# Kernel tuning notes

Measured on AMD Instinct MI355X. Metric: run time of the kernel, lower is better.

The kernel has to match this reference:

```python
import jax, jax.numpy as jnp
import numpy as np

SIGMA_MIN, SIGMA_MAX = 0.03, 0.35
LAMBDA_GEO = 8.0
COMPAT_SCALE = 0.1
INVALID_W = 0.05
NH, HD = 8, 64
LN_EPS = 1e-5

def _ln(x, g, b):
    m = x.mean(-1, keepdims=True)
    v = ((x - m) ** 2).mean(-1, keepdims=True)
    return (x - m) * jax.lax.rsqrt(v + LN_EPS) * g + b

def setup_inputs() -> dict:
    key = jax.random.key(0)
    ks = jax.random.split(key, 32)
    B, C, H, W = 8, 512, 32, 32
    T, S, D, SIN = 1024, 1024, 512, 512
    s = 0.02
    inp = {
        'front_feat': jax.random.normal(ks[0], (B, C, H, W), jnp.float32),
        'sat_tokens': jax.random.normal(ks[1], (B, S, SIN), jnp.float32),
        'sat_xy': jax.random.uniform(ks[2], (B, S, 2), jnp.float32),
        'front_bev_xy': jax.random.uniform(ks[3], (B, T, 2), jnp.float32),
        'front_bev_valid_mask': jax.random.bernoulli(ks[4], 0.9, (B, T)),
        'front_plucker': jax.random.normal(ks[5], (B, T, 6), jnp.float32),
        'fa_w': jax.random.normal(ks[6], (C, D), jnp.float32) * s,
        'fa_b': jnp.zeros((D,), jnp.float32),
        'fa_g': jnp.ones((D,), jnp.float32),
        'fa_lb': jnp.zeros((D,), jnp.float32),
        'sa_w': jax.random.normal(ks[7], (SIN, D), jnp.float32) * s,
        'sa_b': jnp.zeros((D,), jnp.float32),
        'sa_g': jnp.ones((D,), jnp.float32),
        'sa_lb': jnp.zeros((D,), jnp.float32),
        'q_w': jax.random.normal(ks[8], (D, D), jnp.float32) * s,
        'q_b': jnp.zeros((D,), jnp.float32),
        'k_w': jax.random.normal(ks[9], (D, D), jnp.float32) * s,
        'k_b': jnp.zeros((D,), jnp.float32),
        'v_w': jax.random.normal(ks[10], (D, D), jnp.float32) * s,
        'v_b': jnp.zeros((D,), jnp.float32),
        'pl_w1': jax.random.normal(ks[11], (6, D), jnp.float32) * s,
        'pl_b1': jnp.zeros((D,), jnp.float32),
        'pl_w2': jax.random.normal(ks[12], (D, D), jnp.float32) * s,
        'pl_b2': jnp.zeros((D,), jnp.float32),
        'sig_w': jax.random.normal(ks[13], (D, 1), jnp.float32) * s,
        'sig_b': jnp.zeros((1,), jnp.float32),
        'db_w': jax.random.normal(ks[14], (D, NH), jnp.float32) * s,
        'db_b': jnp.zeros((NH,), jnp.float32),
        'out_w': jax.random.normal(ks[15], (D, C), jnp.float32) * s,
        'out_b': jnp.zeros((C,), jnp.float32),
    }
    return inp

def _forward(front_feat, sat_tokens, sat_xy, front_bev_xy, front_plucker,
             fa_w, fa_b, fa_g, fa_lb, sa_w, sa_b, sa_g, sa_lb,
             q_w, q_b, k_w, k_b, v_w, v_b, pl_w1, pl_b1, pl_w2, pl_b2,
             sig_w, sig_b, db_w, db_b, out_w, out_b, valid_mask):
    B, C, H, W = front_feat.shape
    T = H * W
    D = NH * HD
    front_flat = front_feat.reshape(B, C, T).transpose(0, 2, 1)  # [B,T,C]
    front_embed = _ln(front_flat @ fa_w + fa_b, fa_g, fa_lb)
    pl = jax.nn.silu(front_plucker @ pl_w1 + pl_b1) @ pl_w2 + pl_b2
    context = front_embed + pl
    sat_embed = _ln(sat_tokens @ sa_w + sa_b, sa_g, sa_lb)
    def heads(x):
        return x.reshape(B, -1, NH, HD).transpose(0, 2, 1, 3)  # [B,H,N,d]
    q = heads(front_embed @ q_w + q_b)
    k = heads(sat_embed @ k_w + k_b)
    v = heads(sat_embed @ v_w + v_b)
    compat = jnp.einsum('bhtd,bhsd->bhts', q, k) / jnp.sqrt(jnp.float32(HD))
    compat = COMPAT_SCALE * compat
    sigma = SIGMA_MIN + (SIGMA_MAX - SIGMA_MIN) * jax.nn.sigmoid((context @ sig_w + sig_b)[..., 0])  # [B,T]
    dist2 = ((front_bev_xy[:, :, None, :] - sat_xy[:, None, :, :]) ** 2).sum(-1)  # [B,T,S]
    geo = -LAMBDA_GEO * dist2 / jnp.maximum(sigma[..., None] ** 2, 1e-6)
    sat_logits = compat + geo[:, None]  # [B,H,T,S]
    sat_logits = jnp.where(valid_mask[:, None, :, None], sat_logits, jnp.float32(-10000.0))
    dustbin = (context @ db_w + db_b).transpose(0, 2, 1)[..., None]  # [B,H,T,1]
    logits = jnp.concatenate([sat_logits, dustbin], axis=-1)
    probs = jax.nn.softmax(logits, axis=-1)
    sat_probs, dustbin_prob = probs[..., :-1], probs[..., -1]
    read = jnp.einsum('bhts,bhsd->bhtd', sat_probs, v)
    read = read.transpose(0, 2, 1, 3).reshape(B, T, D)
    read_feat = (read @ out_w + out_b).transpose(0, 2, 1).reshape(B, C, H, W)
    confidence = (1.0 - dustbin_prob).mean(axis=1)  # [B,T]
    conf_feat = confidence.reshape(B, 1, H, W)
    front_feat_out = front_feat + conf_feat * read_feat
    vf = valid_mask.astype(confidence.dtype)
    inv = 1.0 - vf
    invalid_conf = (confidence * inv).sum() / jnp.maximum(inv.sum(), 1.0)
    invalid_conf_loss = invalid_conf * INVALID_W
    return front_feat_out, read_feat, confidence, invalid_conf_loss

def reference(front_feat, sat_tokens, sat_xy, front_bev_xy, front_bev_valid_mask, front_plucker,
              fa_w, fa_b, fa_g, fa_lb, sa_w, sa_b, sa_g, sa_lb,
              q_w, q_b, k_w, k_b, v_w, v_b, pl_w1, pl_b1, pl_w2, pl_b2,
              sig_w, sig_b, db_w, db_b, out_w, out_b):
    return _forward(front_feat, sat_tokens, sat_xy, front_bev_xy, front_plucker,
                    fa_w, fa_b, fa_g, fa_lb, sa_w, sa_b, sa_g, sa_lb,
                    q_w, q_b, k_w, k_b, v_w, v_b, pl_w1, pl_b1, pl_w2, pl_b2,
                    sig_w, sig_b, db_w, db_b, out_w, out_b, front_bev_valid_mask)
```

## Files before the change

kernel.cpp:

```cpp
#include <hip/hip_runtime.h>

typedef unsigned short u16;
typedef __attribute__((ext_vector_type(8))) short short8;
typedef __attribute__((ext_vector_type(4))) float f32x4;

constexpr int B_  = 8;
constexpr int C_  = 512;
constexpr int T_  = 1024;
constexpr int S_  = 1024;
constexpr int D_  = 512;
constexpr int NH_ = 8;
constexpr int BT_ = B_ * T_;
constexpr float INVLN2 = 1.44269504088896340736f;
constexpr float QSCALE2 = 0.0125f * INVLN2;

__device__ __forceinline__ unsigned pack2(float lo, float hi) {
    unsigned r;
    asm("v_cvt_pk_bf16_f32 %0, %1, %2" : "=v"(r) : "v"(lo), "v"(hi));
    return r;
}
__device__ __forceinline__ u16 f2bf(float x) {
    return (u16)pack2(x, x);
}
__device__ __forceinline__ float bf2f(u16 h) {
    union { unsigned u; float f; } v; v.u = ((unsigned)h) << 16;
    return v.f;
}
__device__ __forceinline__ float fexp2(float x) {
    float r;
    asm("v_exp_f32 %0, %1" : "=v"(r) : "v"(x));
    return r;
}
__device__ __forceinline__ float max3f(float a, float b, float c) {
    float r;
    asm("v_max3_f32 %0, %1, %2, %3" : "=v"(r) : "v"(a), "v"(b), "v"(c));
    return r;
}

#define GWAITBAR(N) do { \
    asm volatile("s_waitcnt vmcnt(" #N ") lgkmcnt(0)" ::: "memory"); \
    __builtin_amdgcn_sched_barrier(0); \
    __builtin_amdgcn_s_barrier(); \
    __builtin_amdgcn_sched_barrier(0); } while (0)

typedef __attribute__((address_space(3))) unsigned int lds_u32;
typedef const __attribute__((address_space(1))) unsigned int glob_u32;
__device__ __forceinline__ void g2l16(void* l, const void* g) {
    __builtin_amdgcn_global_load_lds((glob_u32*)g, (lds_u32*)l, 16, 0, 0);
}

__device__ __forceinline__ int is_valid(const void* mask, int mode, int idx) {
    if (mode == 0) return ((const int*)mask)[idx] != 0;
    if (mode == 1) return ((const float*)mask)[idx] != 0.0f;
    return ((const unsigned char*)mask)[idx] != 0;
}

__global__ __launch_bounds__(256) void prep_k(
    const float* __restrict__ ff, const float* __restrict__ sat,
    const float* __restrict__ pl,
    const float* a0, const float* a1, const float* a2, const float* a3,
    const float* a4, const float* a5, u16* __restrict__ WT,
    u16* __restrict__ ffb, u16* __restrict__ satb,
    const float* __restrict__ plw1, const float* __restrict__ plb1,
    u16* __restrict__ plh,
    const unsigned* __restrict__ maskw, int* __restrict__ mode,
    float* __restrict__ scal,
    const float* __restrict__ plw2, const float* __restrict__ sigw,
    const float* __restrict__ dbw, const float* __restrict__ plb2,
    float* __restrict__ wsig, float* __restrict__ wdbfT,
    float* __restrict__ offs, float* __restrict__ dbwT) {
    __shared__ float tile[32][33];
    int blk = blockIdx.x, tid = threadIdx.x;
    if (blk < 4096) {
        int t0 = (blk & 31) * 32, c0 = ((blk >> 5) & 15) * 32, b = blk >> 9;
        int tx = tid & 31, ty = tid >> 5;
        const float* ip = ff + (size_t)b * C_ * T_;
        for (int i = ty; i < 32; i += 8)
            tile[i][tx] = ip[(size_t)(c0 + i) * T_ + t0 + tx];
        __syncthreads();
        u16* op = ffb + (size_t)b * T_ * C_;
        for (int i = ty; i < 32; i += 8)
            op[(size_t)(t0 + i) * C_ + c0 + tx] = f2bf(tile[tx][i]);
    } else if (blk < 5632) {
        int idx = blk - 4096;
        const float* srcs[6] = {a0, a1, a2, a3, a4, a5};
        int z = idx >> 8;
        const float* src = srcs[z];
        u16* d = WT + (size_t)z * 512 * 512;
        int k0 = (idx & 15) * 32, n0 = ((idx >> 4) & 15) * 32;
        int tx = tid & 31, ty = tid >> 5;
        for (int i = ty; i < 32; i += 8)
            tile[i][tx] = src[(size_t)(k0 + i) * 512 + n0 + tx];
        __syncthreads();
        for (int i = ty; i < 32; i += 8)
            d[(size_t)(n0 + i) * 512 + k0 + tx] = f2bf(tile[tx][i]);
    } else if (blk < 7680) {
        int i = (blk - 5632) * 256 + tid;
        const float4* p = (const float4*)(sat + (size_t)i * 8);
        float4 a = p[0], b = p[1];
        uint4 o;
        o.x = pack2(a.x, a.y); o.y = pack2(a.z, a.w);
        o.z = pack2(b.x, b.y); o.w = pack2(b.z, b.w);
        *(uint4*)(satb + (size_t)i * 8) = o;
    } else if (blk < 9728) {
        int m = (blk - 7680) * 4 + (tid >> 6);
        int lane = tid & 63;
        float p6[6];
#pragma unroll
        for (int j = 0; j < 6; ++j) p6[j] = pl[(size_t)m * 6 + j];
        int n0 = lane * 8;
        float acc[8];
#pragma unroll
        for (int e = 0; e < 8; ++e) acc[e] = plb1[n0 + e];
#pragma unroll
        for (int j = 0; j < 6; ++j) {
            float4 wv0 = *(const float4*)(plw1 + j * D_ + n0);
            float4 wv1 = *(const float4*)(plw1 + j * D_ + n0 + 4);
            acc[0] += p6[j] * wv0.x; acc[1] += p6[j] * wv0.y;
            acc[2] += p6[j] * wv0.z; acc[3] += p6[j] * wv0.w;
            acc[4] += p6[j] * wv1.x; acc[5] += p6[j] * wv1.y;
            acc[6] += p6[j] * wv1.z; acc[7] += p6[j] * wv1.w;
        }
        uint4 o;
        float s0 = acc[0] / (1.0f + __expf(-acc[0]));
        float s1 = acc[1] / (1.0f + __expf(-acc[1]));
        float s2 = acc[2] / (1.0f + __expf(-acc[2]));
        float s3 = acc[3] / (1.0f + __expf(-acc[3]));
        float s4 = acc[4] / (1.0f + __expf(-acc[4]));
        float s5 = acc[5] / (1.0f + __expf(-acc[5]));
        float s6 = acc[6] / (1.0f + __expf(-acc[6]));
        float s7 = acc[7] / (1.0f + __expf(-acc[7]));
        o.x = pack2(s0, s1); o.y = pack2(s2, s3);
        o.z = pack2(s4, s5); o.w = pack2(s6, s7);
        *(uint4*)(plh + (size_t)m * D_ + n0) = o;
    } else if (blk == 9728) {
        __shared__ int bad_i, bad_f;
        if (tid == 0) { bad_i = 0; bad_f = 0; }
        __syncthreads();
        for (int i = tid; i < 2048; i += 256) {
            unsigned v = maskw[i];
            if (v > 1u) bad_i = 1;
            if (v != 0u && v != 0x3f800000u) bad_f = 1;
        }
        __syncthreads();
        if (tid == 0) {
            *mode = (!bad_i) ? 0 : ((!bad_f) ? 1 : 2);
            scal[0] = 0.0f; scal[1] = 0.0f;
        }
    } else if (blk < 9731) {
        int k = (blk - 9729) * 256 + tid;
        const float* wr = plw2 + (size_t)k * 512;
        float acc = 0;
        for (int n = 0; n < 512; n += 4) {
            float4 wv = *(const float4*)(wr + n);
            float4 sv = *(const float4*)(sigw + n);
            acc += wv.x * sv.x + wv.y * sv.y + wv.z * sv.z + wv.w * sv.w;
        }
        wsig[k] = acc;
    } else if (blk < 9747) {
        int idx = blk - 9731;
        int k = idx * 32 + (tid >> 3), h = tid & 7;
        const float* wr = plw2 + (size_t)k * 512;
        float acc = 0;
        for (int n = 0; n < 512; ++n) acc += wr[n] * dbw[n * 8 + h];
        wdbfT[h * 512 + k] = acc;
    } else if (blk == 9747) {
        float p = plb2[tid] * sigw[tid] + plb2[tid + 256] * sigw[tid + 256];
        float ph[8];
#pragma unroll
        for (int h = 0; h < 8; ++h)
            ph[h] = plb2[tid] * dbw[tid * 8 + h] +
                    plb2[tid + 256] * dbw[(tid + 256) * 8 + h];
        for (int o = 32; o; o >>= 1) {
            p += __shfl_down(p, o);
#pragma unroll
            for (int h = 0; h < 8; ++h) ph[h] += __shfl_down(ph[h], o);
        }
        __shared__ float red[4][9];
        int wv = tid >> 6, lane = tid & 63;
        if (lane == 0) {
            red[wv][0] = p;
#pragma unroll
            for (int h = 0; h < 8; ++h) red[wv][1 + h] = ph[h];
        }
        __syncthreads();
        if (tid == 0) {
            for (int j = 0; j < 9; ++j) {
                float t = 0;
                for (int v2 = 0; v2 < 4; ++v2) t += red[v2][j];
                offs[j] = t;
            }
        }
    } else {
        for (int i = tid; i < 4096; i += 256) {
            int h = i >> 9, n = i & 511;
            dbwT[h * 512 + n] = dbw[n * 8 + h];
        }
    }
}

__global__ __launch_bounds__(256) void gmm_k(
    const u16* __restrict__ A0, const u16* __restrict__ A1,
    const u16* __restrict__ A2, const u16* __restrict__ A3,
    const u16* __restrict__ Bt0, const u16* __restrict__ Bt1,
    const u16* __restrict__ Bt2, const u16* __restrict__ Bt3,
    const float* __restrict__ bb0, const float* __restrict__ bb1,
    const float* __restrict__ bb2, const float* __restrict__ bb3,
    void* __restrict__ C0v, void* __restrict__ C1v,
    void* __restrict__ C2v, void* __restrict__ C3v,
    int md0, int md1, int md2, int md3,
    const u16* __restrict__ addend,
    const float* __restrict__ ffp, float* __restrict__ out1p,
    const float* __restrict__ dbpp, const void* __restrict__ maskp,
    const int* __restrict__ modep, float* __restrict__ outcp,
    float* __restrict__ scalp) {
    __shared__ u16 As[3][4096];
    __shared__ u16 Bs[3][4096];
    __shared__ float confL[128];
    int jid = blockIdx.x >> 8;
    int L = blockIdx.x & 255;
    const u16* A    = (jid == 0) ? A0 : (jid == 1) ? A1 : (jid == 2) ? A2 : A3;
    const u16* Bt   = (jid == 0) ? Bt0 : (jid == 1) ? Bt1 : (jid == 2) ? Bt2 : Bt3;
    const float* bias = (jid == 0) ? bb0 : (jid == 1) ? bb1 : (jid == 2) ? bb2 : bb3;
    void* Cv        = (jid == 0) ? C0v : (jid == 1) ? C1v : (jid == 2) ? C2v : C3v;
    int mode        = (jid == 0) ? md0 : (jid == 1) ? md1 : (jid == 2) ? md2 : md3;

    int tid = threadIdx.x, w = tid >> 6, l = tid & 63;
    int lr = l & 15, g = l >> 4;
    int W = (L & 7) * 32 + (L >> 3);
    int m0 = (W >> 2) * 128, n0 = (W & 3) * 128;
    int wr = w >> 1, wc = w & 1;
    int prm = g ^ ((lr >> 1) & 3);

    f32x4 acc[4][4] = {};

    if (mode == 4 && tid < 128) {
        int row = m0 + tid;
        const float* dr = dbpp + (size_t)row * NH_;
        float s = 0;
#pragma unroll
        for (int h = 0; h < 8; ++h) s += dr[h];
        float cf = 1.0f - s * 0.125f;
        confL[tid] = cf;
        if ((W & 3) == 0) {
            outcp[row] = cf;
            int md = *modep;
            float invd = is_valid(maskp, md, row) ? 0.0f : 1.0f;
            float a = cf * invd, bsum = invd;
            for (int o = 32; o; o >>= 1) {
                a += __shfl_down(a, o);
                bsum += __shfl_down(bsum, o);
            }
            if ((tid & 63) == 0) {
                atomicAdd(&scalp[0], a);
                atomicAdd(&scalp[1], bsum);
            }
        }
    }

    auto stage = [&](int buf, int k0) {
#pragma unroll
        for (int j = 0; j < 2; ++j) {
            int i = tid + 256 * j;
            int row = i >> 2, gg = (i & 3) ^ ((i >> 3) & 3);
            g2l16((char*)As[buf] + (size_t)i * 16,
                  A + (size_t)(m0 + row) * 512 + k0 + gg * 8);
        }
#pragma unroll
        for (int j = 0; j < 2; ++j) {
            int i = tid + 256 * j;
            int col = i >> 2, gg = (i & 3) ^ ((i >> 3) & 3);
            g2l16((char*)Bs[buf] + (size_t)i * 16,
                  Bt + (size_t)(n0 + col) * 512 + k0 + gg * 8);
        }
    };

    auto compute = [&](int bi) {
        const char* Ab = (const char*)As[bi];
        const char* Bb = (const char*)Bs[bi];
        short8 af[4], bf[4];
#pragma unroll
        for (int m = 0; m < 4; ++m)
            af[m] = *(const short8*)(Ab + ((wr * 64 + m * 16 + lr) * 4 + prm) * 16);
#pragma unroll
        for (int n = 0; n < 4; ++n)
            bf[n] = *(const short8*)(Bb + ((wc * 64 + n * 16 + lr) * 4 + prm) * 16);
        __builtin_amdgcn_s_setprio(1);
#pragma unroll
        for (int m = 0; m < 4; ++m)
#pragma unroll
            for (int n = 0; n < 4; ++n)
                acc[m][n] = __builtin_amdgcn_mfma_f32_16x16x32_bf16(
                    af[m], bf[n], acc[m][n], 0, 0, 0);
        __builtin_amdgcn_s_setprio(0);
    };

    stage(0, 0);
    stage(1, 32);
    for (int t = 0; t < 14; ++t) {
        stage((t + 2) % 3, (t + 2) * 32);
        GWAITBAR(8);
        compute(t % 3);
        __builtin_amdgcn_s_barrier();
    }
    GWAITBAR(4);
    compute(2);
    GWAITBAR(0);
    compute(0);

    float bs[4];
#pragma unroll
    for (int n = 0; n < 4; ++n) bs[n] = bias[n0 + wc * 64 + n * 16 + lr];

#pragma unroll
    for (int m = 0; m < 4; ++m) {
#pragma unroll
        for (int n = 0; n < 4; ++n) {
            int R0  = m0 + wr * 64 + m * 16 + 4 * g;
            int col = n0 + wc * 64 + n * 16 + lr;
            if (mode == 3) {
                int bbx = R0 >> 10, ss = R0 & 1023, hh = col >> 6, dd = col & 63;
                uint2 pk;
                pk.x = pack2(acc[m][n][0] + bs[n], acc[m][n][1] + bs[n]);
                pk.y = pack2(acc[m][n][2] + bs[n], acc[m][n][3] + bs[n]);
                u16* dst = (u16*)Cv + ((size_t)(bbx * 8 + hh) * 64 + dd) * 1024 + ss;
                *(uint2*)dst = pk;
            } else if (mode == 4) {
                int bbx = R0 >> 10, t0p = R0 & 1023;
                size_t base = (size_t)bbx * C_ * T_ + (size_t)col * T_ + t0p;
                float4 rf;
                rf.x = acc[m][n][0] + bs[n]; rf.y = acc[m][n][1] + bs[n];
                rf.z = acc[m][n][2] + bs[n]; rf.w = acc[m][n][3] + bs[n];
                float4 ffv = *(const float4*)(ffp + base);
                float4 cfv = *(const float4*)&confL[R0 - m0];
                float4 o0v;
                o0v.x = ffv.x + cfv.x * rf.x; o0v.y = ffv.y + cfv.y * rf.y;
                o0v.z = ffv.z + cfv.z * rf.z; o0v.w = ffv.w + cfv.w * rf.w;
                *(float4*)(out1p + base) = rf;
                *(float4*)((float*)Cv + base) = o0v;
            } else {
#pragma unroll
                for (int j = 0; j < 4; ++j) {
                    int row = R0 + j;
                    float v = acc[m][n][j] + bs[n];
                    if (mode == 1) v *= QSCALE2;
                    if (mode == 2) v += bf2f(addend[(size_t)row * 512 + col]);
                    ((u16*)Cv)[(size_t)row * 512 + col] = f2bf(v);
                }
            }
        }
    }
}

__global__ __launch_bounds__(256) void ln2_k(
    const u16* __restrict__ X0, const float* __restrict__ g0,
    const float* __restrict__ b0, u16* __restrict__ O0,
    const u16* __restrict__ X1, const float* __restrict__ g1,
    const float* __restrict__ b1, u16* __restrict__ O1) {
    int sel = blockIdx.x >> 13;
    int row = blockIdx.x & 8191;
    const u16* X = sel ? X1 : X0;
    const float* gw = sel ? g1 : g0;
    const float* bw = sel ? b1 : b0;
    u16* out = sel ? O1 : O0;
    int tid = threadIdx.x;
    const unsigned* xr = (const unsigned*)(X + (size_t)row * D_);
    unsigned u = xr[tid];
    float x0 = bf2f((u16)(u & 0xffff)), x1 = bf2f((u16)(u >> 16));
    float s = x0 + x1, sq = x0 * x0 + x1 * x1;
    __shared__ float rs[4], rq[4];
    for (int o = 32; o; o >>= 1) { s += __shfl_down(s, o); sq += __shfl_down(sq, o); }
    int wid = tid >> 6, lane = tid & 63;
    if (lane == 0) { rs[wid] = s; rq[wid] = sq; }
    __syncthreads();
    if (tid == 0) {
        float ts = 0, tq = 0;
        for (int w = 0; w < 4; ++w) { ts += rs[w]; tq += rq[w]; }
        rs[0] = ts; rq[0] = tq;
    }
    __syncthreads();
    float mean = rs[0] * (1.0f / D_);
    float var  = rq[0] * (1.0f / D_) - mean * mean;
    float r = rsqrtf(var + 1e-5f);
    float2 g2 = *(const float2*)(gw + 2 * tid);
    float2 b2 = *(const float2*)(bw + 2 * tid);
    float y0 = (x0 - mean) * r * g2.x + b2.x;
    float y1 = (x1 - mean) * r * g2.y + b2.y;
    ((unsigned*)(out + (size_t)row * D_))[tid] = pack2(y0, y1);
}

__global__ __launch_bounds__(256) void head2_k(
    const u16* __restrict__ E, const u16* __restrict__ PLH,
    const float* __restrict__ sigw, const float* __restrict__ sigb,
    const float* __restrict__ wsig, const float* __restrict__ dbwT,
    const float* __restrict__ wdbfT, const float* __restrict__ dbb,
    const float* __restrict__ offs,
    float* __restrict__ sigma, float* __restrict__ dbo) {
    int wv = threadIdx.x >> 6, lane = threadIdx.x & 63;
    int row = blockIdx.x * 4 + wv;
    uint4 ue = *((const uint4*)(E + (size_t)row * 512) + lane);
    float Ev[8];
    Ev[0] = bf2f((u16)(ue.x & 0xffff)); Ev[1] = bf2f((u16)(ue.x >> 16));
    Ev[2] = bf2f((u16)(ue.y & 0xffff)); Ev[3] = bf2f((u16)(ue.y >> 16));
    Ev[4] = bf2f((u16)(ue.z & 0xffff)); Ev[5] = bf2f((u16)(ue.z >> 16));
    Ev[6] = bf2f((u16)(ue.w & 0xffff)); Ev[7] = bf2f((u16)(ue.w >> 16));
    uint4 up = *((const uint4*)(PLH + (size_t)row * 512) + lane);
    float plv[8];
    plv[0] = bf2f((u16)(up.x & 0xffff)); plv[1] = bf2f((u16)(up.x >> 16));
    plv[2] = bf2f((u16)(up.y & 0xffff)); plv[3] = bf2f((u16)(up.y >> 16));
    plv[4] = bf2f((u16)(up.z & 0xffff)); plv[5] = bf2f((u16)(up.z >> 16));
    plv[6] = bf2f((u16)(up.w & 0xffff)); plv[7] = bf2f((u16)(up.w >> 16));

    int n0 = lane * 8;
    float4 sw0 = *(const float4*)(sigw + n0);
    float4 sw1 = *(const float4*)(sigw + n0 + 4);
    float4 fw0 = *(const float4*)(wsig + n0);
    float4 fw1 = *(const float4*)(wsig + n0 + 4);
    float swv[8] = {sw0.x, sw0.y, sw0.z, sw0.w, sw1.x, sw1.y, sw1.z, sw1.w};
    float fwv[8] = {fw0.x, fw0.y, fw0.z, fw0.w, fw1.x, fw1.y, fw1.z, fw1.w};
    float sacc = 0;
#pragma unroll
    for (int i = 0; i < 8; ++i) sacc += Ev[i] * swv[i] + plv[i] * fwv[i];

    float d_[8];
#pragma unroll
    for (int h = 0; h < 8; ++h) {
        const float* ar = dbwT + h * 512 + n0;
        const float* br = wdbfT + h * 512 + n0;
        float4 a0v = *(const float4*)ar;
        float4 a1v = *(const float4*)(ar + 4);
        float4 b0v = *(const float4*)br;
        float4 b1v = *(const float4*)(br + 4);
        d_[h] = Ev[0] * a0v.x + Ev[1] * a0v.y + Ev[2] * a0v.z + Ev[3] * a0v.w +
                Ev[4] * a1v.x + Ev[5] * a1v.y + Ev[6] * a1v.z + Ev[7] * a1v.w +
                plv[0] * b0v.x + plv[1] * b0v.y + plv[2] * b0v.z + plv[3] * b0v.w +
                plv[4] * b1v.x + plv[5] * b1v.y + plv[6] * b1v.z + plv[7] * b1v.w;
    }
    for (int o = 1; o < 64; o <<= 1) {
        sacc += __shfl_xor(sacc, o);
#pragma unroll
        for (int h = 0; h < 8; ++h) d_[h] += __shfl_xor(d_[h], o);
    }
    if (lane == 0) {
        float z = sacc + sigb[0] + offs[0];
        sigma[row] = 0.03f + 0.32f / (1.0f + __expf(-z));
        float* dd = dbo + (size_t)row * NH_;
#pragma unroll
        for (int h = 0; h < 8; ++h) dd[h] = d_[h] + dbb[h] + offs[1 + h];
    }
}

__global__ __launch_bounds__(512) void attn_k(
    const u16* __restrict__ Q, const u16* __restrict__ K,
    const u16* __restrict__ Vt, const float* __restrict__ sig,
    const float* __restrict__ dbl, const float* __restrict__ bev,
    const float* __restrict__ sxy, const void* __restrict__ mask,
    const int* __restrict__ mode, u16* __restrict__ OUT,
    float* __restrict__ dbp) {
    int L = blockIdx.x;
    int W = (L & 7) * 64 + (L >> 3);
    int b = W >> 6, h = (W >> 3) & 7, tblk = W & 7;
    int tid = threadIdx.x, w = tid >> 6, l = tid & 63;
    int lr = l & 15, g = l >> 4;
    int p8 = lr & 7;

    __shared__ u16 Kbuf[2][4096];
    __shared__ u16 Vbuf[2][4096];
    __shared__ float2 SXY[1024];
    __shared__ float  SZ[1024];

    const float2* xp = (const float2*)(sxy + (size_t)b * S_ * 2);
#pragma unroll
    for (int j = 0; j < 2; ++j) {
        int idx = tid + 512 * j;
        float2 v = xp[idx];
        SXY[idx] = make_float2(-2.0f * v.x, -2.0f * v.y);
        SZ[idx] = v.x * v.x + v.y * v.y;
    }

    int trow = b * T_ + tblk * 128 + w * 16 + lr;
    float s_ = sig[trow];
    float bx = bev[(size_t)trow * 2], by = bev[(size_t)trow * 2 + 1];
    float dbv2 = dbl[(size_t)trow * NH_ + h] * INVLN2;
    int md = *mode;
    bool vld = is_valid(mask, md, trow) != 0;
    float grow  = vld ? (-11.5415603271117f / fmaxf(s_ * s_, 1e-6f)) : 0.0f;
    float Abase = vld ? grow * (bx * bx + by * by) : -10000.0f;
    float AbaseM = Abase - dbv2;
    float mshift = 0.0f;

    const u16* qp = Q + (size_t)trow * 512 + h * 64 + g * 8;
    short8 q0 = *(const short8*)qp;
    short8 q1 = *(const short8*)(qp + 32);
    if (!vld) { q0 = short8{}; q1 = short8{}; }

    short8 ones;
#pragma unroll
    for (int e = 0; e < 8; ++e) ones[e] = (short)0x3F80;

    const u16* Kp = K + (size_t)b * S_ * 512 + h * 64;
    const u16* Vp = Vt + (size_t)(b * 8 + h) * 64 * 1024;

    int srow = tid >> 3;
    int gprm = (tid & 7) ^ (srow & 7);
    int sK = ((srow >> 5) & 1) * 32 + ((srow >> 2) & 3) * 8 +
             ((srow >> 4) & 1) * 4 + (srow & 3);

    auto stageKV = [&](int buf, int s0) {
        g2l16((char*)Kbuf[buf] + (size_t)tid * 16,
              Kp + (size_t)(s0 + sK) * 512 + gprm * 8);
        g2l16((char*)Vbuf[buf] + (size_t)tid * 16,
              Vp + (size_t)srow * 1024 + s0 + gprm * 8);
    };

    f32x4 o0 = {}, o1 = {}, o2 = {}, o3 = {};
    f32x4 o4 = {1.0f, 1.0f, 1.0f, 1.0f};

    stageKV(0, 0);
    int cur = 0;
    for (int c = 0; c < 16; ++c) {
        int s0c = c * 64;
        if (c < 15) {
            stageKV(cur ^ 1, s0c + 64);
            GWAITBAR(2);
        } else {
            GWAITBAR(0);
        }

        const char* Kc = (const char*)Kbuf[cur];
        const char* Vc = (const char*)Vbuf[cur];

        f32x4 p[4];
        f32x4 z4 = {};
        __builtin_amdgcn_s_setprio(1);
#pragma unroll
        for (int sub = 0; sub < 4; ++sub) {
            int krow = sub * 16 + lr;
            short8 kf0 = *(const short8*)(Kc + (krow * 8 + (g ^ p8)) * 16);
            short8 kf1 = *(const short8*)(Kc + (krow * 8 + ((4 + g) ^ p8)) * 16);
            p[sub] = __builtin_amdgcn_mfma_f32_16x16x32_bf16(kf0, q0, z4, 0, 0, 0);
            p[sub] = __builtin_amdgcn_mfma_f32_16x16x32_bf16(kf1, q1, p[sub], 0, 0, 0);
        }
        __builtin_amdgcn_s_setprio(0);

        float lg[16];
#pragma unroll
        for (int sub = 0; sub < 4; ++sub) {
            int sl = s0c + ((sub & 2) << 4) + 8 * g + ((sub & 1) << 2);
            float4 xy01 = *(const float4*)&SXY[sl];
            float4 xy23 = *(const float4*)&SXY[sl + 2];
            float4 zz   = *(const float4*)&SZ[sl];
            float X[4] = {xy01.x, xy01.z, xy23.x, xy23.z};
            float Y[4] = {xy01.y, xy01.w, xy23.y, xy23.w};
            float Z[4] = {zz.x, zz.y, zz.z, zz.w};
#pragma unroll
            for (int i2 = 0; i2 < 4; ++i2) {
                float wg = fmaf(bx, X[i2], fmaf(by, Y[i2], Z[i2]));
                lg[sub * 4 + i2] = fmaf(grow, wg, p[sub][i2] + AbaseM);
            }
        }
        float c0 = max3f(lg[0], lg[1], lg[2]);
        float c1 = max3f(lg[3], lg[4], lg[5]);
        float c2 = max3f(lg[6], lg[7], lg[8]);
        float c3 = max3f(lg[9], lg[10], lg[11]);
        float c4 = max3f(lg[12], lg[13], lg[14]);
        float cl = fmaxf(max3f(c0, c1, c2), max3f(c3, c4, lg[15]));

        if (!__all(cl <= 11.5f)) {
            cl = fmaxf(cl, __shfl_xor(cl, 16));
            cl = fmaxf(cl, __shfl_xor(cl, 32));
            float dm = fmaxf(cl, 0.0f);
            float scl = fexp2(-dm);
            o0 *= scl; o1 *= scl; o2 *= scl; o3 *= scl; o4 *= scl;
            AbaseM -= dm;
            mshift -= dm;
#pragma unroll
            for (int r = 0; r < 16; ++r) lg[r] -= dm;
        }
        float pe[16];
#pragma unroll
        for (int r = 0; r < 16; ++r) pe[r] = fexp2(lg[r]);

        union { uint4 u; short8 s8; } pf0, pf1;
        pf0.u.x = pack2(pe[0], pe[1]);  pf0.u.y = pack2(pe[2], pe[3]);
        pf0.u.z = pack2(pe[4], pe[5]);  pf0.u.w = pack2(pe[6], pe[7]);
        pf1.u.x = pack2(pe[8], pe[9]);  pf1.u.y = pack2(pe[10], pe[11]);
        pf1.u.z = pack2(pe[12], pe[13]); pf1.u.w = pack2(pe[14], pe[15]);

        __builtin_amdgcn_s_setprio(1);
        short8 vf;
#pragma unroll
        for (int dt = 0; dt < 4; ++dt) {
            int vrow = dt * 16 + lr;
            f32x4* oo = (dt == 0) ? &o0 : (dt == 1) ? &o1 : (dt == 2) ? &o2 : &o3;
            vf = *(const short8*)(Vc + (vrow * 8 + (g ^ p8)) * 16);
            *oo = __builtin_amdgcn_mfma_f32_16x16x32_bf16(vf, pf0.s8, *oo, 0, 0, 0);
            vf = *(const short8*)(Vc + (vrow * 8 + ((4 + g) ^ p8)) * 16);
            *oo = __builtin_amdgcn_mfma_f32_16x16x32_bf16(vf, pf1.s8, *oo, 0, 0, 0);
        }
        o4 = __builtin_amdgcn_mfma_f32_16x16x32_bf16(ones, pf0.s8, o4, 0, 0, 0);
        o4 = __builtin_amdgcn_mfma_f32_16x16x32_bf16(ones, pf1.s8, o4, 0, 0, 0);
        __builtin_amdgcn_s_setprio(0);

        __builtin_amdgcn_s_barrier();
        cur ^= 1;
    }

    float inv = 1.0f / o4[0];
    u16* ob = OUT + (size_t)trow * 512 + h * 64;
    {
        uint2 pk;
        pk.x = pack2(o0[0] * inv, o0[1] * inv); pk.y = pack2(o0[2] * inv, o0[3] * inv);
        *(uint2*)(ob + 0 * 16 + 4 * g) = pk;
        pk.x = pack2(o1[0] * inv, o1[1] * inv); pk.y = pack2(o1[2] * inv, o1[3] * inv);
        *(uint2*)(ob + 1 * 16 + 4 * g) = pk;
        pk.x = pack2(o2[0] * inv, o2[1] * inv); pk.y = pack2(o2[2] * inv, o2[3] * inv);
        *(uint2*)(ob + 2 * 16 + 4 * g) = pk;
        pk.x = pack2(o3[0] * inv, o3[1] * inv); pk.y = pack2(o3[2] * inv, o3[3] * inv);
        *(uint2*)(ob + 3 * 16 + 4 * g) = pk;
    }
    if (g == 0) dbp[(size_t)trow * NH_ + h] = fexp2(mshift) * inv;
}

__global__ void loss_k(const float* __restrict__ scal, float* __restrict__ out) {
    out[0] = scal[0] / fmaxf(scal[1], 1.0f) * 0.05f;
}

extern "C" void kernel_launch(void* const* d_in, const int* in_sizes, int n_in,
                              void* d_out, int out_size, void* d_ws, size_t ws_size,
                              hipStream_t stream) {
    const float* front_feat = (const float*)d_in[0];
    const float* sat_tokens = (const float*)d_in[1];
    const float* sat_xy     = (const float*)d_in[2];
    const float* bev_xy     = (const float*)d_in[3];
    const void*  mask       = d_in[4];
    const float* plucker    = (const float*)d_in[5];
    const float* fa_w = (const float*)d_in[6];
    const float* fa_b = (const float*)d_in[7];
    const float* fa_g = (const float*)d_in[8];
    const float* fa_lb = (const float*)d_in[9];
    const float* sa_w = (const float*)d_in[10];
    const float* sa_b = (const float*)d_in[11];
    const float* sa_g = (const float*)d_in[12];
    const float* sa_lb = (const float*)d_in[13];
    const float* q_w = (const float*)d_in[14];
    const float* q_b = (const float*)d_in[15];
    const float* k_w = (const float*)d_in[16];
    const float* k_b = (const float*)d_in[17];
    const float* v_w = (const float*)d_in[18];
    const float* v_b = (const float*)d_in[19];
    const float* pl_w1 = (const float*)d_in[20];
    const float* pl_b1 = (const float*)d_in[21];
    const float* pl_w2 = (const float*)d_in[22];
    const float* pl_b2 = (const float*)d_in[23];
    const float* sig_w = (const float*)d_in[24];
    const float* sig_b = (const float*)d_in[25];
    const float* db_w = (const float*)d_in[26];
    const float* db_b = (const float*)d_in[27];
    const float* out_w = (const float*)d_in[28];
    const float* out_b = (const float*)d_in[29];

    char* w8 = (char*)d_ws;
    u16* H0 = (u16*)(w8);
    u16* H1 = (u16*)(w8 + 8388608ull * 1);
    u16* H2 = (u16*)(w8 + 8388608ull * 2);
    u16* H3 = (u16*)(w8 + 8388608ull * 3);
    u16* H4 = (u16*)(w8 + 8388608ull * 4);
    u16* H5 = (u16*)(w8 + 8388608ull * 5);
    u16* H6 = (u16*)(w8 + 8388608ull * 6);
    u16* WT = (u16*)(w8 + 8388608ull * 7);
    char* sm = w8 + 8388608ull * 7 + 3670016ull;
    float* w_sigma = (float*)sm;
    float* w_db    = w_sigma + BT_;
    float* w_dbp   = w_db + (size_t)BT_ * NH_;
    float* w_scal  = w_dbp + (size_t)BT_ * NH_;
    int*   w_mode  = (int*)(w_scal + 2);
    float* w_wsig  = w_scal + 4;
    float* w_wdbfT = w_wsig + 512;
    float* w_offs  = w_wdbfT + 4096;
    float* w_dbwT  = w_offs + 16;

    u16* Wfa = WT;                 u16* Wq  = WT + 262144ull * 1;
    u16* Wsa = WT + 262144ull * 2; u16* Wk  = WT + 262144ull * 3;
    u16* Wv  = WT + 262144ull * 4; u16* Wo  = WT + 262144ull * 5;

    float* out0 = (float*)d_out;
    float* out1 = out0 + (size_t)B_ * C_ * T_;
    float* outc = out1 + (size_t)B_ * C_ * T_;
    float* outl = outc + (size_t)B_ * T_;

    dim3 blk(256);

    prep_k<<<dim3(9749), blk, 0, stream>>>(
        front_feat, sat_tokens, plucker,
        fa_w, q_w, sa_w, k_w, v_w, out_w, WT,
        H0, H5, pl_w1, pl_b1, H2,
        (const unsigned*)mask, w_mode, w_scal,
        pl_w2, sig_w, db_w, pl_b2, w_wsig, w_wdbfT, w_offs, w_dbwT);
    gmm_k<<<dim3(512), blk, 0, stream>>>(
        H0, H5, nullptr, nullptr,
        Wfa, Wsa, nullptr, nullptr,
        fa_b, sa_b, nullptr, nullptr,
        H6, H4, nullptr, nullptr,
        0, 0, 0, 0,
        nullptr, nullptr, nullptr,
        nullptr, nullptr, nullptr, nullptr, nullptr);
    ln2_k<<<dim3(16384), blk, 0, stream>>>(H6, fa_g, fa_lb, H1,
                                           H4, sa_g, sa_lb, H3);
    head2_k<<<dim3(2048), blk, 0, stream>>>(
        H1, H2, sig_w, sig_b, w_wsig, w_dbwT, w_wdbfT, db_b, w_offs,
        w_sigma, w_db);
    gmm_k<<<dim3(768), blk, 0, stream>>>(
        H1, H3, H3, nullptr,
        Wq, Wk, Wv, nullptr,
        q_b, k_b, v_b, nullptr,
        H5, H0, H4, nullptr,
        1, 0, 3, 0,
        nullptr, nullptr, nullptr,
        nullptr, nullptr, nullptr, nullptr, nullptr);
    attn_k<<<dim3(512), dim3(512), 0, stream>>>(
        H5, H0, H4, w_sigma, w_db, bev_xy, sat_xy, mask, w_mode, H2, w_dbp);
    gmm_k<<<dim3(256), blk, 0, stream>>>(
        H2, nullptr, nullptr, nullptr,
        Wo, nullptr, nullptr, nullptr,
        out_b, nullptr, nullptr, nullptr,
        out0, nullptr, nullptr, nullptr,
        4, 0, 0, 0,
        nullptr, front_feat, out1,
        w_dbp, mask, w_mode, outc, w_scal);
    loss_k<<<1, 1, 0, stream>>>(w_scal, outl);
}
```

Before: 156.6 us.

## Fuse head projection into LayerNorm and split output GEMM into narrower tiles

The sigma and dustbin head computation is folded into the LayerNorm kernel, so the normalized front features are used directly from registers instead of being reread by a separate head kernel, and one launch is dropped. The final output projection moves from the generic GEMM kernel to a dedicated kernel with 128x64 tiles and 512 blocks, doubling the block count to fill more compute units. In exchange, each LN block gains extra reductions and a barrier, and the narrower tiles reread A more often. The generic GEMM loses its unused mode-2 and mode-4 paths.

Result: no change. 159.7 us (+2.0%).

```diff
diff --git a/kernel.cpp b/kernel.cpp
--- a/kernel.cpp
+++ b/kernel.cpp
@@ -201,29 +201,22 @@
 
 __global__ __launch_bounds__(256) void gmm_k(
     const u16* __restrict__ A0, const u16* __restrict__ A1,
-    const u16* __restrict__ A2, const u16* __restrict__ A3,
+    const u16* __restrict__ A2,
     const u16* __restrict__ Bt0, const u16* __restrict__ Bt1,
-    const u16* __restrict__ Bt2, const u16* __restrict__ Bt3,
+    const u16* __restrict__ Bt2,
     const float* __restrict__ bb0, const float* __restrict__ bb1,
-    const float* __restrict__ bb2, const float* __restrict__ bb3,
-    void* __restrict__ C0v, void* __restrict__ C1v,
-    void* __restrict__ C2v, void* __restrict__ C3v,
-    int md0, int md1, int md2, int md3,
-    const u16* __restrict__ addend,
-    const float* __restrict__ ffp, float* __restrict__ out1p,
-    const float* __restrict__ dbpp, const void* __restrict__ maskp,
-    const int* __restrict__ modep, float* __restrict__ outcp,
-    float* __restrict__ scalp) {
+    const float* __restrict__ bb2,
+    void* __restrict__ C0v, void* __restrict__ C1v, void* __restrict__ C2v,
+    int md0, int md1, int md2) {
     __shared__ u16 As[3][4096];
     __shared__ u16 Bs[3][4096];
-    __shared__ float confL[128];
     int jid = blockIdx.x >> 8;
     int L = blockIdx.x & 255;
-    const u16* A    = (jid == 0) ? A0 : (jid == 1) ? A1 : (jid == 2) ? A2 : A3;
-    const u16* Bt   = (jid == 0) ? Bt0 : (jid == 1) ? Bt1 : (jid == 2) ? Bt2 : Bt3;
-    const float* bias = (jid == 0) ? bb0 : (jid == 1) ? bb1 : (jid == 2) ? bb2 : bb3;
-    void* Cv        = (jid == 0) ? C0v : (jid == 1) ? C1v : (jid == 2) ? C2v : C3v;
-    int mode        = (jid == 0) ? md0 : (jid == 1) ? md1 : (jid == 2) ? md2 : md3;
+    const u16* A    = (jid == 0) ? A0 : (jid == 1) ? A1 : A2;
+    const u16* Bt   = (jid == 0) ? Bt0 : (jid == 1) ? Bt1 : Bt2;
+    const float* bias = (jid == 0) ? bb0 : (jid == 1) ? bb1 : bb2;
+    void* Cv        = (jid == 0) ? C0v : (jid == 1) ? C1v : C2v;
+    int mode        = (jid == 0) ? md0 : (jid == 1) ? md1 : md2;
 
     int tid = threadIdx.x, w = tid >> 6, l = tid & 63;
     int lr = l & 15, g = l >> 4;
@@ -234,7 +227,107 @@
 
     f32x4 acc[4][4] = {};
 
-    if (mode == 4 && tid < 128) {
+    auto stage = [&](int buf, int k0) {
+#pragma unroll
+        for (int j = 0; j < 2; ++j) {
+            int i = tid + 256 * j;
+            int row = i >> 2, gg = (i & 3) ^ ((i >> 3) & 3);
+            g2l16((char*)As[buf] + (size_t)i * 16,
+                  A + (size_t)(m0 + row) * 512 + k0 + gg * 8);
+        }
+#pragma unroll
+        for (int j = 0; j < 2; ++j) {
+            int i = tid + 256 * j;
+            int col = i >> 2, gg = (i & 3) ^ ((i >> 3) & 3);
+            g2l16((char*)Bs[buf] + (size_t)i * 16,
+                  Bt + (size_t)(n0 + col) * 512 + k0 + gg * 8);
+        }
+    };
+
+    auto compute = [&](int bi) {
+        const char* Ab = (const char*)As[bi];
+        const char* Bb = (const char*)Bs[bi];
+        short8 af[4], bf[4];
+#pragma unroll
+        for (int m = 0; m < 4; ++m)
+            af[m] = *(const short8*)(Ab + ((wr * 64 + m * 16 + lr) * 4 + prm) * 16);
+#pragma unroll
+        for (int n = 0; n < 4; ++n)
+            bf[n] = *(const short8*)(Bb + ((wc * 64 + n * 16 + lr) * 4 + prm) * 16);
+        __builtin_amdgcn_s_setprio(1);
+#pragma unroll
+        for (int m = 0; m < 4; ++m)
+#pragma unroll
+            for (int n = 0; n < 4; ++n)
+                acc[m][n] = __builtin_amdgcn_mfma_f32_16x16x32_bf16(
+                    af[m], bf[n], acc[m][n], 0, 0, 0);
+        __builtin_amdgcn_s_setprio(0);
+    };
+
+    stage(0, 0);
+    stage(1, 32);
+    for (int t = 0; t < 14; ++t) {
+        stage((t + 2) % 3, (t + 2) * 32);
+        GWAITBAR(8);
+        compute(t % 3);
+        __builtin_amdgcn_s_barrier();
+    }
+    GWAITBAR(4);
+    compute(2);
+    GWAITBAR(0);
+    compute(0);
+
+    float bs[4];
+#pragma unroll
+    for (int n = 0; n < 4; ++n) bs[n] = bias[n0 + wc * 64 + n * 16 + lr];
+
+#pragma unroll
+    for (int m = 0; m < 4; ++m) {
+#pragma unroll
+        for (int n = 0; n < 4; ++n) {
+            int R0  = m0 + wr * 64 + m * 16 + 4 * g;
+            int col = n0 + wc * 64 + n * 16 + lr;
+            if (mode == 3) {
+                int bbx = R0 >> 10, ss = R0 & 1023, hh = col >> 6, dd = col & 63;
+                uint2 pk;
+                pk.x = pack2(acc[m][n][0] + bs[n], acc[m][n][1] + bs[n]);
+                pk.y = pack2(acc[m][n][2] + bs[n], acc[m][n][3] + bs[n]);
+                u16* dst = (u16*)Cv + ((size_t)(bbx * 8 + hh) * 64 + dd) * 1024 + ss;
+                *(uint2*)dst = pk;
+            } else {
+#pragma unroll
+                for (int j = 0; j < 4; ++j) {
+                    int row = R0 + j;
+                    float v = acc[m][n][j] + bs[n];
+                    if (mode == 1) v *= QSCALE2;
+                    ((u16*)Cv)[(size_t)row * 512 + col] = f2bf(v);
+                }
+            }
+        }
+    }
+}
+
+__global__ __launch_bounds__(256) void rf64_k(
+    const u16* __restrict__ A, const u16* __restrict__ Bt,
+    const float* __restrict__ bias, float* __restrict__ out0,
+    const float* __restrict__ ffp, float* __restrict__ out1p,
+    const float* __restrict__ dbpp, const void* __restrict__ maskp,
+    const int* __restrict__ modep, float* __restrict__ outcp,
+    float* __restrict__ scalp) {
+    __shared__ u16 As[3][4096];
+    __shared__ u16 Bs[3][2048];
+    __shared__ float confL[128];
+    int L = blockIdx.x;
+    int W = (L & 7) * 64 + (L >> 3);
+    int m0 = (W >> 3) * 128, n0 = (W & 7) * 64;
+    int tid = threadIdx.x, w = tid >> 6, l = tid & 63;
+    int lr = l & 15, g = l >> 4;
+    int wr = w >> 1, wc = w & 1;
+    int prm = g ^ ((lr >> 1) & 3);
+
+    f32x4 acc[4][2] = {};
+
+    if (tid < 128) {
         int row = m0 + tid;
         const float* dr = dbpp + (size_t)row * NH_;
         float s = 0;
@@ -242,7 +335,7 @@
         for (int h = 0; h < 8; ++h) s += dr[h];
         float cf = 1.0f - s * 0.125f;
         confL[tid] = cf;
-        if ((W & 3) == 0) {
+        if ((W & 7) == 0) {
             outcp[row] = cf;
             int md = *modep;
             float invd = is_valid(maskp, md, row) ? 0.0f : 1.0f;
@@ -266,11 +359,9 @@
             g2l16((char*)As[buf] + (size_t)i * 16,
                   A + (size_t)(m0 + row) * 512 + k0 + gg * 8);
         }
-#pragma unroll
-        for (int j = 0; j < 2; ++j) {
-            int i = tid + 256 * j;
-            int col = i >> 2, gg = (i & 3) ^ ((i >> 3) & 3);
-            g2l16((char*)Bs[buf] + (size_t)i * 16,
+        {
+            int col = tid >> 2, gg = (tid & 3) ^ ((tid >> 3) & 3);
+            g2l16((char*)Bs[buf] + (size_t)tid * 16,
                   Bt + (size_t)(n0 + col) * 512 + k0 + gg * 8);
         }
     };
@@ -278,18 +369,18 @@
     auto compute = [&](int bi) {
         const char* Ab = (const char*)As[bi];
         const char* Bb = (const char*)Bs[bi];
-        short8 af[4], bf[4];
+        short8 af[4], bf[2];
 #pragma unroll
         for (int m = 0; m < 4; ++m)
             af[m] = *(const short8*)(Ab + ((wr * 64 + m * 16 + lr) * 4 + prm) * 16);
 #pragma unroll
-        for (int n = 0; n < 4; ++n)
-            bf[n] = *(const short8*)(Bb + ((wc * 64 + n * 16 + lr) * 4 + prm) * 16);
+        for (int n = 0; n < 2; ++n)
+            bf[n] = *(const short8*)(Bb + ((wc * 32 + n * 16 + lr) * 4 + prm) * 16);
         __builtin_amdgcn_s_setprio(1);
 #pragma unroll
         for (int m = 0; m < 4; ++m)
 #pragma unroll
-            for (int n = 0; n < 4; ++n)
+            for (int n = 0; n < 2; ++n)
                 acc[m][n] = __builtin_amdgcn_mfma_f32_16x16x32_bf16(
                     af[m], bf[n], acc[m][n], 0, 0, 0);
         __builtin_amdgcn_s_setprio(0);
@@ -299,64 +390,48 @@
     stage(1, 32);
     for (int t = 0; t < 14; ++t) {
         stage((t + 2) % 3, (t + 2) * 32);
-        GWAITBAR(8);
+        GWAITBAR(6);
         compute(t % 3);
         __builtin_amdgcn_s_barrier();
     }
-    GWAITBAR(4);
+    GWAITBAR(3);
     compute(2);
     GWAITBAR(0);
     compute(0);
 
-    float bs[4];
-#pragma unroll
-    for (int n = 0; n < 4; ++n) bs[n] = bias[n0 + wc * 64 + n * 16 + lr];
-
-#pragma unroll
-    for (int m = 0; m < 4; ++m) {
-#pragma unroll
-        for (int n = 0; n < 4; ++n) {
+    float bs[2] = {bias[n0 + wc * 32 + lr], bias[n0 + wc * 32 + 16 + lr]};
+#pragma unroll
+    for (int m = 0; m < 4; ++m)
+#pragma unroll
+        for (int n = 0; n < 2; ++n) {
             int R0  = m0 + wr * 64 + m * 16 + 4 * g;
-            int col = n0 + wc * 64 + n * 16 + lr;
-            if (mode == 3) {
-                int bbx = R0 >> 10, ss = R0 & 1023, hh = col >> 6, dd = col & 63;
-                uint2 pk;
-                pk.x = pack2(acc[m][n][0] + bs[n], acc[m][n][1] + bs[n]);
-                pk.y = pack2(acc[m][n][2] + bs[n], acc[m][n][3] + bs[n]);
-                u16* dst = (u16*)Cv + ((size_t)(bbx * 8 + hh) * 64 + dd) * 1024 + ss;
-                *(uint2*)dst = pk;
-            } else if (mode == 4) {
-                int bbx = R0 >> 10, t0p = R0 & 1023;
-                size_t base = (size_t)bbx * C_ * T_ + (size_t)col * T_ + t0p;
-                float4 rf;
-                rf.x = acc[m][n][0] + bs[n]; rf.y = acc[m][n][1] + bs[n];
-                rf.z = acc[m][n][2] + bs[n]; rf.w = acc[m][n][3] + bs[n];
-                float4 ffv = *(const float4*)(ffp + base);
-                float4 cfv = *(const float4*)&confL[R0 - m0];
-                float4 o0v;
-                o0v.x = ffv.x + cfv.x * rf.x; o0v.y = ffv.y + cfv.y * rf.y;
-                o0v.z = ffv.z + cfv.z * rf.z; o0v.w = ffv.w + cfv.w * rf.w;
-                *(float4*)(out1p + base) = rf;
-                *(float4*)((float*)Cv + base) = o0v;
-            } else {
-#pragma unroll
-                for (int j = 0; j < 4; ++j) {
-                    int row = R0 + j;
-                    float v = acc[m][n][j] + bs[n];
-                    if (mode == 1) v *= QSCALE2;
-                    if (mode == 2) v += bf2f(addend[(size_t)row * 512 + col]);
-                    ((u16*)Cv)[(size_t)row * 512 + col] = f2bf(v);
-                }
-            }
-        }
-    }
-}
-
-__global__ __launch_bounds__(256) void ln2_k(
+            int col = n0 + wc * 32 + n * 16 + lr;
+            int bbx = R0 >> 10, t0p = R0 & 1023;
+            size_t base = (size_t)bbx * C_ * T_ + (size_t)col * T_ + t0p;
+            float4 rf;
+            rf.x = acc[m][n][0] + bs[n]; rf.y = acc[m][n][1] + bs[n];
+            rf.z = acc[m][n][2] + bs[n]; rf.w = acc[m][n][3] + bs[n];
+            float4 ffv = *(const float4*)(ffp + base);
+            float4 cfv = *(const float4*)&confL[R0 - m0];
+            float4 o0v;
+            o0v.x = ffv.x + cfv.x * rf.x; o0v.y = ffv.y + cfv.y * rf.y;
+            o0v.z = ffv.z + cfv.z * rf.z; o0v.w = ffv.w + cfv.w * rf.w;
+            *(float4*)(out1p + base) = rf;
+            *(float4*)(out0 + base) = o0v;
+        }
+}
+
+__global__ __launch_bounds__(256) void ln2h_k(
     const u16* __restrict__ X0, const float* __restrict__ g0,
     const float* __restrict__ b0, u16* __restrict__ O0,
     const u16* __restrict__ X1, const float* __restrict__ g1,
-    const float* __restrict__ b1, u16* __restrict__ O1) {
+    const float* __restrict__ b1, u16* __restrict__ O1,
+    const u16* __restrict__ PLH,
+    const float* __restrict__ sigw, const float* __restrict__ sigb,
+    const float* __restrict__ wsig, const float* __restrict__ dbwT,
+    const float* __restrict__ wdbfT, const float* __restrict__ dbb,
+    const float* __restrict__ offs,
+    float* __restrict__ sigma, float* __restrict__ dbo) {
     int sel = blockIdx.x >> 13;
     int row = blockIdx.x & 8191;
     const u16* X = sel ? X1 : X0;
@@ -369,6 +444,7 @@
     float x0 = bf2f((u16)(u & 0xffff)), x1 = bf2f((u16)(u >> 16));
     float s = x0 + x1, sq = x0 * x0 + x1 * x1;
     __shared__ float rs[4], rq[4];
+    __shared__ float hred[4][9];
     for (int o = 32; o; o >>= 1) { s += __shfl_down(s, o); sq += __shfl_down(sq, o); }
     int wid = tid >> 6, lane = tid & 63;
     if (lane == 0) { rs[wid] = s; rq[wid] = sq; }
@@ -387,66 +463,43 @@
     float y0 = (x0 - mean) * r * g2.x + b2.x;
     float y1 = (x1 - mean) * r * g2.y + b2.y;
     ((unsigned*)(out + (size_t)row * D_))[tid] = pack2(y0, y1);
-}
-
-__global__ __launch_bounds__(256) void head2_k(
-    const u16* __restrict__ E, const u16* __restrict__ PLH,
-    const float* __restrict__ sigw, const float* __restrict__ sigb,
-    const float* __restrict__ wsig, const float* __restrict__ dbwT,
-    const float* __restrict__ wdbfT, const float* __restrict__ dbb,
-    const float* __restrict__ offs,
-    float* __restrict__ sigma, float* __restrict__ dbo) {
-    int wv = threadIdx.x >> 6, lane = threadIdx.x & 63;
-    int row = blockIdx.x * 4 + wv;
-    uint4 ue = *((const uint4*)(E + (size_t)row * 512) + lane);
-    float Ev[8];
-    Ev[0] = bf2f((u16)(ue.x & 0xffff)); Ev[1] = bf2f((u16)(ue.x >> 16));
-    Ev[2] = bf2f((u16)(ue.y & 0xffff)); Ev[3] = bf2f((u16)(ue.y >> 16));
-    Ev[4] = bf2f((u16)(ue.z & 0xffff)); Ev[5] = bf2f((u16)(ue.z >> 16));
-    Ev[6] = bf2f((u16)(ue.w & 0xffff)); Ev[7] = bf2f((u16)(ue.w >> 16));
-    uint4 up = *((const uint4*)(PLH + (size_t)row * 512) + lane);
-    float plv[8];
-    plv[0] = bf2f((u16)(up.x & 0xffff)); plv[1] = bf2f((u16)(up.x >> 16));
-    plv[2] = bf2f((u16)(up.y & 0xffff)); plv[3] = bf2f((u16)(up.y >> 16));
-    plv[4] = bf2f((u16)(up.z & 0xffff)); plv[5] = bf2f((u16)(up.z >> 16));
-    plv[6] = bf2f((u16)(up.w & 0xffff)); plv[7] = bf2f((u16)(up.w >> 16));
-
-    int n0 = lane * 8;
-    float4 sw0 = *(const float4*)(sigw + n0);
-    float4 sw1 = *(const float4*)(sigw + n0 + 4);
-    float4 fw0 = *(const float4*)(wsig + n0);
-    float4 fw1 = *(const float4*)(wsig + n0 + 4);
-    float swv[8] = {sw0.x, sw0.y, sw0.z, sw0.w, sw1.x, sw1.y, sw1.z, sw1.w};
-    float fwv[8] = {fw0.x, fw0.y, fw0.z, fw0.w, fw1.x, fw1.y, fw1.z, fw1.w};
-    float sacc = 0;
-#pragma unroll
-    for (int i = 0; i < 8; ++i) sacc += Ev[i] * swv[i] + plv[i] * fwv[i];
-
-    float d_[8];
-#pragma unroll
-    for (int h = 0; h < 8; ++h) {
-        const float* ar = dbwT + h * 512 + n0;
-        const float* br = wdbfT + h * 512 + n0;
-        float4 a0v = *(const float4*)ar;
-        float4 a1v = *(const float4*)(ar + 4);
-        float4 b0v = *(const float4*)br;
-        float4 b1v = *(const float4*)(br + 4);
-        d_[h] = Ev[0] * a0v.x + Ev[1] * a0v.y + Ev[2] * a0v.z + Ev[3] * a0v.w +
-                Ev[4] * a1v.x + Ev[5] * a1v.y + Ev[6] * a1v.z + Ev[7] * a1v.w +
-                plv[0] * b0v.x + plv[1] * b0v.y + plv[2] * b0v.z + plv[3] * b0v.w +
-                plv[4] * b1v.x + plv[5] * b1v.y + plv[6] * b1v.z + plv[7] * b1v.w;
-    }
-    for (int o = 1; o < 64; o <<= 1) {
-        sacc += __shfl_xor(sacc, o);
-#pragma unroll
-        for (int h = 0; h < 8; ++h) d_[h] += __shfl_xor(d_[h], o);
-    }
-    if (lane == 0) {
-        float z = sacc + sigb[0] + offs[0];
-        sigma[row] = 0.03f + 0.32f / (1.0f + __expf(-z));
-        float* dd = dbo + (size_t)row * NH_;
-#pragma unroll
-        for (int h = 0; h < 8; ++h) dd[h] = d_[h] + dbb[h] + offs[1 + h];
+
+    if (sel == 0) {
+        unsigned upl = ((const unsigned*)(PLH + (size_t)row * D_))[tid];
+        float pl0 = bf2f((u16)(upl & 0xffff)), pl1 = bf2f((u16)(upl >> 16));
+        float2 sw = *(const float2*)(sigw + 2 * tid);
+        float2 fw = *(const float2*)(wsig + 2 * tid);
+        float sacc = y0 * sw.x + y1 * sw.y + pl0 * fw.x + pl1 * fw.y;
+        float d_[8];
+#pragma unroll
+        for (int h = 0; h < 8; ++h) {
+            float2 av = *(const float2*)(dbwT + h * 512 + 2 * tid);
+            float2 bv = *(const float2*)(wdbfT + h * 512 + 2 * tid);
+            d_[h] = y0 * av.x + y1 * av.y + pl0 * bv.x + pl1 * bv.y;
+        }
+        for (int o = 32; o; o >>= 1) {
+            sacc += __shfl_down(sacc, o);
+#pragma unroll
+            for (int h = 0; h < 8; ++h) d_[h] += __shfl_down(d_[h], o);
+        }
+        if (lane == 0) {
+            hred[wid][0] = sacc;
+#pragma unroll
+            for (int h = 0; h < 8; ++h) hred[wid][1 + h] = d_[h];
+        }
+        __syncthreads();
+        if (tid == 0) {
+            float t0 = hred[0][0] + hred[1][0] + hred[2][0] + hred[3][0];
+            float z = t0 + sigb[0] + offs[0];
+            sigma[row] = 0.03f + 0.32f / (1.0f + __expf(-z));
+            float* dd = dbo + (size_t)row * NH_;
+#pragma unroll
+            for (int h = 0; h < 8; ++h) {
+                float th = hred[0][1 + h] + hred[1][1 + h] +
+                           hred[2][1 + h] + hred[3][1 + h];
+                dd[h] = th + dbb[h] + offs[1 + h];
+            }
+        }
     }
 }
 
@@ -698,35 +751,26 @@
         (const unsigned*)mask, w_mode, w_scal,
         pl_w2, sig_w, db_w, pl_b2, w_wsig, w_wdbfT, w_offs, w_dbwT);
     gmm_k<<<dim3(512), blk, 0, stream>>>(
-        H0, H5, nullptr, nullptr,
-        Wfa, Wsa, nullptr, nullptr,
-        fa_b, sa_b, nullptr, nullptr,
-        H6, H4, nullptr, nullptr,
-        0, 0, 0, 0,
-        nullptr, nullptr, nullptr,
-        nullptr, nullptr, nullptr, nullptr, nullptr);
-    ln2_k<<<dim3(16384), blk, 0, stream>>>(H6, fa_g, fa_lb, H1,
-                                           H4, sa_g, sa_lb, H3);
-    head2_k<<<dim3(2048), blk, 0, stream>>>(
-        H1, H2, sig_w, sig_b, w_wsig, w_dbwT, w_wdbfT, db_b, w_offs,
+        H0, H5, nullptr,
+        Wfa, Wsa, nullptr,
+        fa_b, sa_b, nullptr,
+        H6, H4, nullptr,
+        0, 0, 0);
+    ln2h_k<<<dim3(16384), blk, 0, stream>>>(
+        H6, fa_g, fa_lb, H1,
+        H4, sa_g, sa_lb, H3,
+        H2, sig_w, sig_b, w_wsig, w_dbwT, w_wdbfT, db_b, w_offs,
         w_sigma, w_db);
     gmm_k<<<dim3(768), blk, 0, stream>>>(
-        H1, H3, H3, nullptr,
-        Wq, Wk, Wv, nullptr,
-        q_b, k_b, v_b, nullptr,
-        H5, H0, H4, nullptr,
-        1, 0, 3, 0,
-        nullptr, nullptr, nullptr,
-        nullptr, nullptr, nullptr, nullptr, nullptr);
+        H1, H3, H3,
+        Wq, Wk, Wv,
+        q_b, k_b, v_b,
+        H5, H0, H4,
+        1, 0, 3);
     attn_k<<<dim3(512), dim3(512), 0, stream>>>(
         H5, H0, H4, w_sigma, w_db, bev_xy, sat_xy, mask, w_mode, H2, w_dbp);
-    gmm_k<<<dim3(256), blk, 0, stream>>>(
-        H2, nullptr, nullptr, nullptr,
-        Wo, nullptr, nullptr, nullptr,
-        out_b, nullptr, nullptr, nullptr,
-        out0, nullptr, nullptr, nullptr,
-        4, 0, 0, 0,
-        nullptr, front_feat, out1,
+    rf64_k<<<dim3(512), blk, 0, stream>>>(
+        H2, Wo, out_b, out0, front_feat, out1,
         w_dbp, mask, w_mode, outc, w_scal);
     loss_k<<<1, 1, 0, stream>>>(w_scal, outl);
 }
```
